# Kernel tuning notes

Measured on AMD Instinct MI355X. Metric: run time of the kernel, lower is better.

The kernel has to match this reference:

```python
import jax, jax.numpy as jnp
import numpy as np

N_NODES = 100000
N_EDGES = 640000
D_FEAT = 128
UNITS = 128


def setup_inputs() -> dict:
    key = jax.random.key(0)
    k1, k2, k3, k4, k5 = jax.random.split(key, 5)
    X = jax.random.normal(k1, (N_NODES, D_FEAT), dtype=jnp.float32)
    ref_A = jax.random.randint(k2, (N_EDGES,), 0, N_NODES, dtype=jnp.int32)
    ref_B = jax.random.randint(k3, (N_EDGES,), 0, N_NODES, dtype=jnp.int32)
    # GlorotUniform-style params (scale approximated; exact init irrelevant for math)
    limit_w = np.sqrt(6.0 / (D_FEAT + UNITS)).astype(np.float32)
    w = jax.random.uniform(k4, (D_FEAT, UNITS), minval=-limit_w, maxval=limit_w, dtype=jnp.float32)
    b = jax.random.uniform(k5, (UNITS,), minval=-0.1, maxval=0.1, dtype=jnp.float32)
    return {"X": X, "ref_A": ref_A, "ref_B": ref_B, "w": w, "b": b}


def reference(X, ref_A, ref_B, w, b):
    # c.convolution: gather source-node features along edges, scatter-add to
    # destination nodes (sum aggregation over incoming messages).
    msgs = X[ref_A]                                        # [E, D]
    agg = jax.ops.segment_sum(msgs, ref_B, num_segments=X.shape[0])  # [N, D]
    out = agg @ w + b                                      # [N, units]
    return out
```

## Files before the change

### kernel.cpp

```cpp
#include <hip/hip_runtime.h>
#include <hip/hip_bf16.h>

typedef short s16x8 __attribute__((ext_vector_type(8)));
typedef float f32x4 __attribute__((ext_vector_type(4)));

#define CAPN 32

static __device__ inline unsigned short f2bf(float f) {
    __hip_bfloat16 h = __float2bfloat16(f);
    return *reinterpret_cast<unsigned short*>(&h);
}
static __device__ inline float bf2f(unsigned short u) {
    return __uint_as_float((unsigned int)u << 16);
}

__global__ __launch_bounds__(256) void zwt_kernel(
    const float* __restrict__ w, unsigned short* __restrict__ wTh,
    unsigned short* __restrict__ wTl, int* __restrict__ cnt, int Ncap)
{
    int i = blockIdx.x * 256 + threadIdx.x;
    if (i < Ncap) cnt[i] = 0;
    if (i < 16384) {
        int n = i >> 7, k = i & 127;
        float v = w[k * 128 + n];
        unsigned short hi = f2bf(v);
        wTh[i] = hi;
        wTl[i] = f2bf(v - bf2f(hi));
    }
}

__global__ __launch_bounds__(256) void bingemm_kernel(
    const float* __restrict__ X, const int* __restrict__ A,
    const int* __restrict__ B, const unsigned short* __restrict__ wTh,
    const unsigned short* __restrict__ wTl, int* __restrict__ cnt,
    unsigned int* __restrict__ entries, unsigned short* __restrict__ Yh,
    int N, int E)
{
    const int tid = threadIdx.x;

    const int e0 = blockIdx.x * 512 + tid;
    const int e1 = e0 + 256;
    const bool v0 = (e0 < E), v1 = (e1 < E);
    int a0 = 0, d0 = 0, a1 = 0, d1 = 0;
    if (v0) { a0 = A[e0]; d0 = B[e0]; }
    if (v1) { a1 = A[e1]; d1 = B[e1]; }

    const int u    = tid >> 6;
    const int lane = tid & 63;
    const int m    = lane & 15;
    const int q    = lane >> 4;
    const int r0   = blockIdx.x * 64;
    const int row  = r0 + u * 16 + m;
    const int rldr = (row < N) ? row : (N - 1);

    f32x4 acc[8] = {};
    #pragma unroll
    for (int s = 0; s < 4; ++s) {
        const float* xr = X + (size_t)rldr * 128 + s * 32 + q * 8;
        float4 x0 = *(const float4*)xr;
        float4 x1 = *(const float4*)(xr + 4);
        float xv[8] = {x0.x, x0.y, x0.z, x0.w, x1.x, x1.y, x1.z, x1.w};
        s16x8 ahi, alo;
        #pragma unroll
        for (int j = 0; j < 8; ++j) {
            unsigned short h = f2bf(xv[j]);
            ahi[j] = (short)h;
            alo[j] = (short)f2bf(xv[j] - bf2f(h));
        }
        #pragma unroll
        for (int c = 0; c < 8; ++c) {
            const size_t wo = (size_t)(c * 16 + m) * 128 + s * 32 + q * 8;
            s16x8 bh = *(const s16x8*)&wTh[wo];
            s16x8 bl = *(const s16x8*)&wTl[wo];
            acc[c] = __builtin_amdgcn_mfma_f32_16x16x32_bf16(ahi, bh, acc[c], 0, 0, 0);
            acc[c] = __builtin_amdgcn_mfma_f32_16x16x32_bf16(alo, bh, acc[c], 0, 0, 0);
            acc[c] = __builtin_amdgcn_mfma_f32_16x16x32_bf16(ahi, bl, acc[c], 0, 0, 0);
        }
    }

    const int r0g = r0 + u * 16 + q * 4;
    #pragma unroll
    for (int c = 0; c < 8; ++c) {
        int col = c * 16 + m;
        #pragma unroll
        for (int r = 0; r < 4; ++r) {
            int orow = r0g + r;
            if (orow < N)
                Yh[(size_t)orow * 128 + col] = f2bf(acc[c][r]);
        }
    }

    if (v0) {
        int p = atomicAdd(&cnt[d0], 1);
        if (p < CAPN) entries[(size_t)d0 * CAPN + p] = (unsigned int)a0;
    }
    if (v1) {
        int p = atomicAdd(&cnt[d1], 1);
        if (p < CAPN) entries[(size_t)d1 * CAPN + p] = (unsigned int)a1;
    }
    for (int e = gridDim.x * 512 + blockIdx.x * 256 + tid; e < E;
         e += gridDim.x * 256) {
        int a = A[e], d = B[e];
        int p = atomicAdd(&cnt[d], 1);
        if (p < CAPN) entries[(size_t)d * CAPN + p] = (unsigned int)a;
    }
}

__global__ __launch_bounds__(256) void gather_kernel(
    const int* __restrict__ cnt, const unsigned int* __restrict__ entries,
    const unsigned short* __restrict__ Yh, const float* __restrict__ b,
    float* __restrict__ out, int N)
{
    const int tid  = threadIdx.x;
    const int u    = tid >> 6;
    const int lane = tid & 63;
    const int nodeBase = blockIdx.x * 16 + u * 4;

    int deg[4];
    {
        int4 d4 = ((const int4*)cnt)[blockIdx.x * 4 + u];
        deg[0] = d4.x; deg[1] = d4.y; deg[2] = d4.z; deg[3] = d4.w;
    }
    int idxl[4], last[4];
    #pragma unroll
    for (int t = 0; t < 4; ++t) {
        int node = nodeBase + t;
        int dg = (node < N) ? min(deg[t], CAPN) : 0;
        deg[t] = dg;
        last[t] = (dg > 0) ? dg - 1 : 0;
        idxl[t] = (lane < dg) ? (int)entries[(size_t)node * CAPN + lane] : 0;
    }

    const int maxdg = max(max(deg[0], deg[1]), max(deg[2], deg[3]));
    const int maxch = (maxdg + 7) >> 3;
    float ax[4] = {0.f, 0.f, 0.f, 0.f};
    float ay[4] = {0.f, 0.f, 0.f, 0.f};
    #pragma unroll 1
    for (int ch = 0; ch < maxch; ++ch) {
        const int base = ch * 8;
        unsigned int p[4][8];
        #pragma unroll
        for (int t = 0; t < 4; ++t) {
            #pragma unroll
            for (int j = 0; j < 8; ++j) {
                int sl = base + j;
                if (sl > last[t]) sl = last[t];
                int s = __shfl(idxl[t], sl);
                p[t][j] = *(const unsigned int*)(Yh + (size_t)s * 128 + lane * 2);
            }
        }
        #pragma unroll
        for (int t = 0; t < 4; ++t) {
            #pragma unroll
            for (int j = 0; j < 8; ++j)
                if (base + j < deg[t]) {
                    ax[t] += __uint_as_float(p[t][j] << 16);
                    ay[t] += __uint_as_float(p[t][j] & 0xFFFF0000u);
                }
        }
    }

    const float2 bb = ((const float2*)b)[lane];
    #pragma unroll
    for (int t = 0; t < 4; ++t) {
        int node = nodeBase + t;
        if (node < N) {
            float2 o = {ax[t] + bb.x, ay[t] + bb.y};
            ((float2*)(out + (size_t)node * 128))[lane] = o;
        }
    }
}

extern "C" void kernel_launch(void* const* d_in, const int* in_sizes, int n_in,
                              void* d_out, int out_size, void* d_ws, size_t ws_size,
                              hipStream_t stream) {
    const float* X = (const float*)d_in[0];
    const int*   A = (const int*)d_in[1];
    const int*   B = (const int*)d_in[2];
    const float* w = (const float*)d_in[3];
    const float* b = (const float*)d_in[4];
    float* out = (float*)d_out;

    const int N = in_sizes[0] / 128;
    const int E = in_sizes[1];
    const int Ncap = (N + 15) & ~15;

    char* wsb = (char*)d_ws;
    size_t off = 0;
    int* cnt = (int*)(wsb + off); off += (size_t)4 * Ncap;
    off = (off + 255) & ~(size_t)255;
    unsigned short* wTh = (unsigned short*)(wsb + off); off += 32768;
    unsigned short* wTl = (unsigned short*)(wsb + off); off += 32768;
    unsigned int* entries = (unsigned int*)(wsb + off); off += (size_t)N * CAPN * 4;
    off = (off + 255) & ~(size_t)255;
    unsigned short* Yh = (unsigned short*)(wsb + off);

    const int zItems = (Ncap > 16384) ? Ncap : 16384;
    zwt_kernel<<<(zItems + 255) / 256, 256, 0, stream>>>(w, wTh, wTl, cnt, Ncap);

    const int GB = (N + 63) / 64;
    bingemm_kernel<<<GB, 256, 0, stream>>>(X, A, B, wTh, wTl, cnt, entries, Yh, N, E);

    gather_kernel<<<(N + 15) / 16, 256, 0, stream>>>(cnt, entries, Yh, b, out, N);
}
```

Baseline: 217.3 us.

## Pad atomic counters apart, widen gather loads to 8 bytes, memset counters

Spaces the per-node atomic counters by a stride of up to 16 ints so concurrent atomics from different destinations fall in different cache lines, with the stride chosen to fit the workspace size. The gather kernel now splits each wave into two half-waves that each load 8-byte chunks of a neighbor row for alternating edges, then combines the halves with a cross-lane shuffle and writes float4 outputs. Counter zeroing moves from the weight-transpose kernel to hipMemsetAsync. The padded counters use more memory and memset traffic, and the degree reads in gather are no longer vectorized.

```diff
diff --git a/kernel.cpp b/kernel.cpp
--- a/kernel.cpp
+++ b/kernel.cpp
@@ -16,10 +16,9 @@
 
 __global__ __launch_bounds__(256) void zwt_kernel(
     const float* __restrict__ w, unsigned short* __restrict__ wTh,
-    unsigned short* __restrict__ wTl, int* __restrict__ cnt, int Ncap)
+    unsigned short* __restrict__ wTl)
 {
     int i = blockIdx.x * 256 + threadIdx.x;
-    if (i < Ncap) cnt[i] = 0;
     if (i < 16384) {
         int n = i >> 7, k = i & 127;
         float v = w[k * 128 + n];
@@ -34,7 +33,7 @@
     const int* __restrict__ B, const unsigned short* __restrict__ wTh,
     const unsigned short* __restrict__ wTl, int* __restrict__ cnt,
     unsigned int* __restrict__ entries, unsigned short* __restrict__ Yh,
-    int N, int E)
+    int N, int E, int sh)
 {
     const int tid = threadIdx.x;
 
@@ -91,17 +90,17 @@
     }
 
     if (v0) {
-        int p = atomicAdd(&cnt[d0], 1);
+        int p = atomicAdd(&cnt[(size_t)d0 << sh], 1);
         if (p < CAPN) entries[(size_t)d0 * CAPN + p] = (unsigned int)a0;
     }
     if (v1) {
-        int p = atomicAdd(&cnt[d1], 1);
+        int p = atomicAdd(&cnt[(size_t)d1 << sh], 1);
         if (p < CAPN) entries[(size_t)d1 * CAPN + p] = (unsigned int)a1;
     }
     for (int e = gridDim.x * 512 + blockIdx.x * 256 + tid; e < E;
          e += gridDim.x * 256) {
         int a = A[e], d = B[e];
-        int p = atomicAdd(&cnt[d], 1);
+        int p = atomicAdd(&cnt[(size_t)d << sh], 1);
         if (p < CAPN) entries[(size_t)d * CAPN + p] = (unsigned int)a;
     }
 }
@@ -109,64 +108,74 @@
 __global__ __launch_bounds__(256) void gather_kernel(
     const int* __restrict__ cnt, const unsigned int* __restrict__ entries,
     const unsigned short* __restrict__ Yh, const float* __restrict__ b,
-    float* __restrict__ out, int N)
+    float* __restrict__ out, int N, int sh)
 {
     const int tid  = threadIdx.x;
     const int u    = tid >> 6;
     const int lane = tid & 63;
+    const int c    = lane & 31;
+    const int h    = lane >> 5;
     const int nodeBase = blockIdx.x * 16 + u * 4;
 
-    int deg[4];
-    {
-        int4 d4 = ((const int4*)cnt)[blockIdx.x * 4 + u];
-        deg[0] = d4.x; deg[1] = d4.y; deg[2] = d4.z; deg[3] = d4.w;
-    }
-    int idxl[4], last[4];
+    int deg[4], idxl[4], last[4];
     #pragma unroll
     for (int t = 0; t < 4; ++t) {
         int node = nodeBase + t;
-        int dg = (node < N) ? min(deg[t], CAPN) : 0;
-        deg[t] = dg;
+        int dg = (node < N) ? min(cnt[(size_t)node << sh], CAPN) : 0;
+        deg[t]  = dg;
         last[t] = (dg > 0) ? dg - 1 : 0;
         idxl[t] = (lane < dg) ? (int)entries[(size_t)node * CAPN + lane] : 0;
     }
 
     const int maxdg = max(max(deg[0], deg[1]), max(deg[2], deg[3]));
     const int maxch = (maxdg + 7) >> 3;
-    float ax[4] = {0.f, 0.f, 0.f, 0.f};
-    float ay[4] = {0.f, 0.f, 0.f, 0.f};
+    float acc[4][4] = {};
     #pragma unroll 1
     for (int ch = 0; ch < maxch; ++ch) {
         const int base = ch * 8;
-        unsigned int p[4][8];
+        uint2 p[4][4];
         #pragma unroll
         for (int t = 0; t < 4; ++t) {
             #pragma unroll
-            for (int j = 0; j < 8; ++j) {
-                int sl = base + j;
+            for (int j = 0; j < 4; ++j) {
+                int sl = base + 2 * j + h;
                 if (sl > last[t]) sl = last[t];
                 int s = __shfl(idxl[t], sl);
-                p[t][j] = *(const unsigned int*)(Yh + (size_t)s * 128 + lane * 2);
+                p[t][j] = *(const uint2*)(Yh + (size_t)s * 128 + c * 4);
             }
         }
         #pragma unroll
         for (int t = 0; t < 4; ++t) {
             #pragma unroll
-            for (int j = 0; j < 8; ++j)
-                if (base + j < deg[t]) {
-                    ax[t] += __uint_as_float(p[t][j] << 16);
-                    ay[t] += __uint_as_float(p[t][j] & 0xFFFF0000u);
-                }
-        }
-    }
-
-    const float2 bb = ((const float2*)b)[lane];
-    #pragma unroll
-    for (int t = 0; t < 4; ++t) {
+            for (int j = 0; j < 4; ++j) {
+                bool ok = (base + 2 * j + h) < deg[t];
+                float f0 = __uint_as_float(p[t][j].x << 16);
+                float f1 = __uint_as_float(p[t][j].x & 0xFFFF0000u);
+                float f2 = __uint_as_float(p[t][j].y << 16);
+                float f3 = __uint_as_float(p[t][j].y & 0xFFFF0000u);
+                acc[t][0] += ok ? f0 : 0.f;
+                acc[t][1] += ok ? f1 : 0.f;
+                acc[t][2] += ok ? f2 : 0.f;
+                acc[t][3] += ok ? f3 : 0.f;
+            }
+        }
+    }
+
+    #pragma unroll
+    for (int t = 0; t < 4; ++t)
+        #pragma unroll
+        for (int k = 0; k < 4; ++k)
+            acc[t][k] += __shfl_xor(acc[t][k], 32);
+
+    const float4 b4 = ((const float4*)b)[c];
+    #pragma unroll
+    for (int tt = 0; tt < 2; ++tt) {
+        int t = h * 2 + tt;
         int node = nodeBase + t;
         if (node < N) {
-            float2 o = {ax[t] + bb.x, ay[t] + bb.y};
-            ((float2*)(out + (size_t)node * 128))[lane] = o;
+            float4 o = {acc[t][0] + b4.x, acc[t][1] + b4.y,
+                        acc[t][2] + b4.z, acc[t][3] + b4.w};
+            ((float4*)(out + (size_t)node * 128))[c] = o;
         }
     }
 }
@@ -185,9 +194,13 @@
     const int E = in_sizes[1];
     const int Ncap = (N + 15) & ~15;
 
+    const size_t fixed = 65536 + (size_t)N * CAPN * 4 + (size_t)N * 128 * 2 + 1024;
+    int sh = 4;
+    while (sh > 0 && ((size_t)Ncap * 4 << sh) + fixed > ws_size) --sh;
+
     char* wsb = (char*)d_ws;
     size_t off = 0;
-    int* cnt = (int*)(wsb + off); off += (size_t)4 * Ncap;
+    int* cnt = (int*)(wsb + off); off += ((size_t)Ncap * 4) << sh;
     off = (off + 255) & ~(size_t)255;
     unsigned short* wTh = (unsigned short*)(wsb + off); off += 32768;
     unsigned short* wTl = (unsigned short*)(wsb + off); off += 32768;
@@ -195,11 +208,12 @@
     off = (off + 255) & ~(size_t)255;
     unsigned short* Yh = (unsigned short*)(wsb + off);
 
-    const int zItems = (Ncap > 16384) ? Ncap : 16384;
-    zwt_kernel<<<(zItems + 255) / 256, 256, 0, stream>>>(w, wTh, wTl, cnt, Ncap);
+    hipMemsetAsync(cnt, 0, ((size_t)Ncap * 4) << sh, stream);
+    zwt_kernel<<<64, 256, 0, stream>>>(w, wTh, wTl);
 
     const int GB = (N + 63) / 64;
-    bingemm_kernel<<<GB, 256, 0, stream>>>(X, A, B, wTh, wTl, cnt, entries, Yh, N, E);
-
-    gather_kernel<<<(N + 15) / 16, 256, 0, stream>>>(cnt, entries, Yh, b, out, N);
-}
+    bingemm_kernel<<<GB, 256, 0, stream>>>(X, A, B, wTh, wTl, cnt, entries, Yh,
+                                           N, E, sh);
+
+    gather_kernel<<<(N + 15) / 16, 256, 0, stream>>>(cnt, entries, Yh, b, out, N, sh);
+}
```

After: 232.2 us. +6.9%, slower.
